# Optimization experiments

Measured on AMD Instinct MI355X. Metric: run time of the kernel, lower is better.

Reference implementation:

```python
import jax, jax.numpy as jnp
import numpy as np

N, E, DIM, H = 50000, 800000, 64, 2
HD = H * DIM


def setup_inputs() -> dict:
    key = jax.random.key(0)
    ks = jax.random.split(key, 16)
    s = 0.05
    return {
        "x": jax.random.normal(ks[0], (N, DIM), jnp.float32),
        "edge_index": jax.random.randint(ks[1], (2, E), 0, N, jnp.int64),
        "Wq": jax.random.normal(ks[2], (DIM, HD), jnp.float32) * s,
        "bq": jax.random.normal(ks[3], (HD,), jnp.float32) * s,
        "Wk": jax.random.normal(ks[4], (DIM, HD), jnp.float32) * s,
        "bk": jax.random.normal(ks[5], (HD,), jnp.float32) * s,
        "Wv": jax.random.normal(ks[6], (DIM, HD), jnp.float32) * s,
        "bv": jax.random.normal(ks[7], (HD,), jnp.float32) * s,
        "Wskip": jax.random.normal(ks[8], (DIM, HD), jnp.float32) * s,
        "bskip": jax.random.normal(ks[9], (HD,), jnp.float32) * s,
        "Wc": jax.random.normal(ks[10], (HD, DIM), jnp.float32) * s,
        "bc": jax.random.normal(ks[11], (DIM,), jnp.float32) * s,
        "gamma": jnp.ones((DIM,), jnp.float32),
        "beta": jnp.zeros((DIM,), jnp.float32),
    }


def reference(x, edge_index, Wq, bq, Wk, bk, Wv, bv, Wskip, bskip, Wc, bc, gamma, beta):
    src, dst = edge_index[0], edge_index[1]  # messages flow src -> dst
    # TransformerConv: per-head q/k/v projections, [N, H, D]
    q = (x @ Wq + bq).reshape(N, H, DIM)
    k = (x @ Wk + bk).reshape(N, H, DIM)
    v = (x @ Wv + bv).reshape(N, H, DIM)
    scale = 1.0 / np.sqrt(DIM).astype(np.float32)
    # edge-wise attention logits: [E, H]
    alpha = jnp.einsum('ehd,ehd->eh', q[dst], k[src]) * scale
    # segment softmax over incoming edges of each dst node (PyG softmax)
    amax = jax.ops.segment_max(alpha, dst, num_segments=N)
    a = jnp.exp(alpha - amax[dst])
    asum = jax.ops.segment_sum(a, dst, num_segments=N)
    a = a / (asum[dst] + 1e-16)
    # weighted scatter-aggregate of values: [N, H, D] -> concat heads
    out = jax.ops.segment_sum(a[:, :, None] * v[src], dst, num_segments=N)
    out = out.reshape(N, HD)
    # root/skip connection (root_weight=True default)
    out = out + (x @ Wskip + bskip)
    # concat linear: H*D -> dim
    out = out @ Wc + bc
    # pyg.LayerNorm default mode='graph': normalize over ALL nodes+features
    out = out - out.mean()
    out = out / (out.std() + 1e-5)  # std with unbiased=False (jnp default ddof=0)
    return out * gamma + beta
```

## Files before the change

### kernel.cpp

```cpp
#include <hip/hip_runtime.h>
#include <hip/hip_bf16.h>

#define N_NODES 50000
#define N_EDGES 800000
#define DIM 64
#define NHEAD 2
#define HD 128
#define NCOL 448
#define MAXDEG 64
#define DEGS 16

#define PREP_B 112
#define EDGE_B 3125
#define PROJ_B 782

typedef short bf16x8 __attribute__((ext_vector_type(8)));
typedef float f32x16 __attribute__((ext_vector_type(16)));
typedef float f32x2 __attribute__((ext_vector_type(2)));

__device__ __forceinline__ unsigned short f2bf(float f) {
    unsigned u = __float_as_uint(f);
    unsigned r = (u + 0x7fffu + ((u >> 16) & 1u)) >> 16;
    return (unsigned short)r;
}
__device__ __forceinline__ unsigned char f2fp8(float f) {
    int r = __builtin_amdgcn_cvt_pk_fp8_f32(f, f, 0, false);
    return (unsigned char)(r & 0xff);
}

__global__ __launch_bounds__(256) void k_prep(
    const float* __restrict__ Wq, const float* __restrict__ bq,
    const float* __restrict__ Wk, const float* __restrict__ bk,
    const float* __restrict__ Wv, const float* __restrict__ bv,
    const float* __restrict__ Wskip, const float* __restrict__ bskip,
    const float* __restrict__ Wc, const float* __restrict__ bc,
    unsigned short* __restrict__ WallT, float* __restrict__ ball,
    double* __restrict__ stats)
{
    int gid = blockIdx.x * 256 + threadIdx.x;
    if (gid == 0) { stats[0] = 0.0; stats[1] = 0.0; }
    const int j = gid >> 6;
    const int d = gid & 63;
    float w, bb;
    if (j < 128) {
        w = Wq[d * HD + j] * 0.125f;
        bb = bq[j] * 0.125f;
    } else if (j < 256) {
        int jj = j - 128;
        w = Wk[d * HD + jj];
        bb = bk[jj];
    } else if (j < 384) {
        int jj = j - 256;
        int h = jj >> 6, jc = jj & 63;
        float s = 0.f, sb = 0.f;
        for (int c = 0; c < 64; c++) {
            float wc = Wc[(h * 64 + c) * DIM + jc];
            s  += Wv[d * HD + h * 64 + c] * wc;
            sb += bv[h * 64 + c] * wc;
        }
        w = s; bb = sb;
    } else {
        int jj = j - 384;
        float s = 0.f, sb = bc[jj];
        for (int c = 0; c < HD; c++) {
            float wc = Wc[c * DIM + jj];
            s  += Wskip[d * HD + c] * wc;
            sb += bskip[c] * wc;
        }
        w = s; bb = sb;
    }
    WallT[gid] = f2bf(w);
    if (d == 0) ball[j] = bb;
}

__global__ __launch_bounds__(256) void k_ep(
    const float* __restrict__ x, const int* __restrict__ ei,
    const unsigned short* __restrict__ WallT, const float* __restrict__ ball,
    float* __restrict__ q, unsigned char* __restrict__ kv, float* __restrict__ skipc,
    int* __restrict__ deg, int* __restrict__ elist)
{
    const int blk = blockIdx.x;
    const int t = threadIdx.x;
    if (blk >= PROJ_B) {
        int gid = (blk - PROJ_B) * 256 + t;
        int src = ei[gid];
        int d   = ei[N_EDGES + gid];
        int pos = atomicAdd(&deg[(size_t)d * DEGS], 1);
        if (pos < MAXDEG) elist[(size_t)d * MAXDEG + pos] = src;
        return;
    }
    const int w = t >> 6;
    const int lane = t & 63;
    const int col = lane & 31;
    const int khalf = lane >> 5;
    const int n0 = blk * 64 + (w >> 1) * 32;
    const int ct0 = (w & 1) * 7;
    const int rowbase = 4 * khalf;

    int nread = n0 + col; if (nread >= N_NODES) nread = N_NODES - 1;
    const float* ap = x + (size_t)nread * 64 + khalf * 8;
    bf16x8 afrag[4];
#pragma unroll
    for (int kk = 0; kk < 4; kk++) {
        float4 xa = *((const float4*)(ap + kk * 16));
        float4 xb4 = *((const float4*)(ap + kk * 16 + 4));
        bf16x8 f;
        f[0] = (short)f2bf(xa.x); f[1] = (short)f2bf(xa.y);
        f[2] = (short)f2bf(xa.z); f[3] = (short)f2bf(xa.w);
        f[4] = (short)f2bf(xb4.x); f[5] = (short)f2bf(xb4.y);
        f[6] = (short)f2bf(xb4.z); f[7] = (short)f2bf(xb4.w);
        afrag[kk] = f;
    }

    for (int tt = 0; tt < 7; tt++) {
        const int gc = (ct0 + tt) * 32 + col;
        const float b = ball[gc];
        f32x16 acc;
#pragma unroll
        for (int r = 0; r < 16; r++) acc[r] = b;
        const unsigned short* bp = WallT + (size_t)gc * 64 + khalf * 8;
#pragma unroll
        for (int kk = 0; kk < 4; kk++) {
            bf16x8 bfrag = *((const bf16x8*)(bp + kk * 16));
            acc = __builtin_amdgcn_mfma_f32_32x32x16_bf16(afrag[kk], bfrag, acc, 0, 0, 0);
        }
        if (gc < 128) {
#pragma unroll
            for (int r = 0; r < 16; r++) {
                int node = n0 + (r & 3) + 8 * (r >> 2) + rowbase;
                if (node < N_NODES) q[(size_t)node * HD + gc] = acc[r];
            }
        } else if (gc < 384) {
            int ch = gc - 128;
#pragma unroll
            for (int r = 0; r < 16; r++) {
                int node = n0 + (r & 3) + 8 * (r >> 2) + rowbase;
                if (node < N_NODES) kv[(size_t)node * 256 + ch] = f2fp8(acc[r]);
            }
        } else {
#pragma unroll
            for (int r = 0; r < 16; r++) {
                int node = n0 + (r & 3) + 8 * (r >> 2) + rowbase;
                if (node < N_NODES) skipc[(size_t)node * DIM + (gc - 384)] = acc[r];
            }
        }
    }
}

__global__ __launch_bounds__(256) void k_attn(
    const float* __restrict__ q, const unsigned char* __restrict__ kv,
    const float* __restrict__ skipc,
    const int* __restrict__ deg, const int* __restrict__ elist,
    float* __restrict__ out, float* __restrict__ parts)
{
    const int w = threadIdx.x >> 6;
    const int lane = threadIdx.x & 63;
    const int g = lane >> 3;
    const int j = lane & 7;
    const int n = blockIdx.x * 4 + w;
    const float4* qp = (const float4*)(q + (size_t)n * HD);
    const float4 qa = qp[2 * j],      qb = qp[2 * j + 1];
    const float4 qc = qp[16 + 2 * j], qd = qp[17 + 2 * j];
    float acc0[8], acc1[8];
#pragma unroll
    for (int i = 0; i < 8; i++) { acc0[i] = 0.f; acc1[i] = 0.f; }
    float l0 = 0.f, l1 = 0.f;
    const int start = n * MAXDEG;
    int dg = deg[(size_t)n * DEGS]; if (dg > MAXDEG) dg = MAXDEG;
    const int end = start + dg;
    for (int b0 = start; b0 < end; b0 += 8) {
        int idx = b0 + g;
        bool valid = idx < end;
        int s = elist[valid ? idx : start];
        const uint2* kp = (const uint2*)(kv + (size_t)s * 256);
        uint2 K0 = kp[j], K1 = kp[8 + j];
        uint2 V0 = kp[16 + j], V1 = kp[24 + j];
        f32x2 k0a = __builtin_amdgcn_cvt_pk_f32_fp8(K0.x, false);
        f32x2 k0b = __builtin_amdgcn_cvt_pk_f32_fp8(K0.x, true);
        f32x2 k0c = __builtin_amdgcn_cvt_pk_f32_fp8(K0.y, false);
        f32x2 k0d = __builtin_amdgcn_cvt_pk_f32_fp8(K0.y, true);
        f32x2 k1a = __builtin_amdgcn_cvt_pk_f32_fp8(K1.x, false);
        f32x2 k1b = __builtin_amdgcn_cvt_pk_f32_fp8(K1.x, true);
        f32x2 k1c = __builtin_amdgcn_cvt_pk_f32_fp8(K1.y, false);
        f32x2 k1d = __builtin_amdgcn_cvt_pk_f32_fp8(K1.y, true);
        float p0 = qa.x * k0a[0] + qa.y * k0a[1] + qa.z * k0b[0] + qa.w * k0b[1]
                 + qb.x * k0c[0] + qb.y * k0c[1] + qb.z * k0d[0] + qb.w * k0d[1];
        float p1 = qc.x * k1a[0] + qc.y * k1a[1] + qc.z * k1b[0] + qc.w * k1b[1]
                 + qd.x * k1c[0] + qd.y * k1c[1] + qd.z * k1d[0] + qd.w * k1d[1];
#pragma unroll
        for (int off = 1; off < 8; off <<= 1) {
            p0 += __shfl_xor(p0, off, 64);
            p1 += __shfl_xor(p1, off, 64);
        }
        float w0 = valid ? __expf(p0) : 0.f;
        float w1 = valid ? __expf(p1) : 0.f;
        l0 += w0; l1 += w1;
        f32x2 v0a = __builtin_amdgcn_cvt_pk_f32_fp8(V0.x, false);
        f32x2 v0b = __builtin_amdgcn_cvt_pk_f32_fp8(V0.x, true);
        f32x2 v0c = __builtin_amdgcn_cvt_pk_f32_fp8(V0.y, false);
        f32x2 v0d = __builtin_amdgcn_cvt_pk_f32_fp8(V0.y, true);
        f32x2 v1a = __builtin_amdgcn_cvt_pk_f32_fp8(V1.x, false);
        f32x2 v1b = __builtin_amdgcn_cvt_pk_f32_fp8(V1.x, true);
        f32x2 v1c = __builtin_amdgcn_cvt_pk_f32_fp8(V1.y, false);
        f32x2 v1d = __builtin_amdgcn_cvt_pk_f32_fp8(V1.y, true);
        acc0[0] += w0 * v0a[0]; acc0[1] += w0 * v0a[1];
        acc0[2] += w0 * v0b[0]; acc0[3] += w0 * v0b[1];
        acc0[4] += w0 * v0c[0]; acc0[5] += w0 * v0c[1];
        acc0[6] += w0 * v0d[0]; acc0[7] += w0 * v0d[1];
        acc1[0] += w1 * v1a[0]; acc1[1] += w1 * v1a[1];
        acc1[2] += w1 * v1b[0]; acc1[3] += w1 * v1b[1];
        acc1[4] += w1 * v1c[0]; acc1[5] += w1 * v1c[1];
        acc1[6] += w1 * v1d[0]; acc1[7] += w1 * v1d[1];
    }
#pragma unroll
    for (int off = 8; off < 64; off <<= 1) {
        l0 += __shfl_xor(l0, off, 64);
        l1 += __shfl_xor(l1, off, 64);
#pragma unroll
        for (int i = 0; i < 8; i++) {
            acc0[i] += __shfl_xor(acc0[i], off, 64);
            acc1[i] += __shfl_xor(acc1[i], off, 64);
        }
    }
    if (g == 0) {
        float inv0 = 1.f / (l0 + 1e-16f), inv1 = 1.f / (l1 + 1e-16f);
        const float4* sk = (const float4*)(skipc + (size_t)n * DIM);
        float4 sa = sk[2 * j], sb = sk[2 * j + 1];
        float o[8];
        o[0] = acc0[0] * inv0 + acc1[0] * inv1 + sa.x;
        o[1] = acc0[1] * inv0 + acc1[1] * inv1 + sa.y;
        o[2] = acc0[2] * inv0 + acc1[2] * inv1 + sa.z;
        o[3] = acc0[3] * inv0 + acc1[3] * inv1 + sa.w;
        o[4] = acc0[4] * inv0 + acc1[4] * inv1 + sb.x;
        o[5] = acc0[5] * inv0 + acc1[5] * inv1 + sb.y;
        o[6] = acc0[6] * inv0 + acc1[6] * inv1 + sb.z;
        o[7] = acc0[7] * inv0 + acc1[7] * inv1 + sb.w;
        float4 r0 = {o[0], o[1], o[2], o[3]}, r1 = {o[4], o[5], o[6], o[7]};
        float4* op = (float4*)(out + (size_t)n * DIM);
        op[2 * j] = r0; op[2 * j + 1] = r1;
        float s_ = 0.f, ss = 0.f;
#pragma unroll
        for (int i = 0; i < 8; i++) { s_ += o[i]; ss += o[i] * o[i]; }
#pragma unroll
        for (int off = 1; off < 8; off <<= 1) {
            s_ += __shfl_xor(s_, off, 64);
            ss += __shfl_xor(ss, off, 64);
        }
        if (j == 0) { parts[n * 2 + 0] = s_; parts[n * 2 + 1] = ss; }
    }
}

#define RED_BLOCKS 100
__global__ __launch_bounds__(256) void k_reduce(
    const float* __restrict__ parts, double* __restrict__ stats)
{
    double s = 0.0, ss = 0.0;
    for (int i = blockIdx.x * 256 + threadIdx.x; i < N_NODES; i += RED_BLOCKS * 256) {
        s  += (double)parts[i * 2 + 0];
        ss += (double)parts[i * 2 + 1];
    }
#pragma unroll
    for (int off = 32; off > 0; off >>= 1) {
        s  += __shfl_down(s, off);
        ss += __shfl_down(ss, off);
    }
    __shared__ double sdd[8];
    int wave = threadIdx.x >> 6;
    if ((threadIdx.x & 63) == 0) { sdd[wave * 2] = s; sdd[wave * 2 + 1] = ss; }
    __syncthreads();
    if (threadIdx.x == 0) {
        double S = 0.0, SS = 0.0;
        for (int w = 0; w < 4; w++) { S += sdd[w * 2]; SS += sdd[w * 2 + 1]; }
        atomicAdd(&stats[0], S);
        atomicAdd(&stats[1], SS);
    }
}

__global__ __launch_bounds__(256) void k_norm(
    float* __restrict__ out, const double* __restrict__ stats,
    const float* __restrict__ gamma, const float* __restrict__ beta)
{
    int i = blockIdx.x * 256 + threadIdx.x;
    if (i >= N_NODES * DIM / 4) return;
    const double cnt = (double)N_NODES * (double)DIM;
    double mean = stats[0] / cnt;
    double var  = stats[1] / cnt - mean * mean;
    if (var < 0.0) var = 0.0;
    float mf = (float)mean;
    float inv = 1.0f / ((float)sqrt(var) + 1e-5f);
    float4 v = ((const float4*)out)[i];
    float4 gv = ((const float4*)gamma)[i & 15];
    float4 bv2 = ((const float4*)beta)[i & 15];
    v.x = (v.x - mf) * inv * gv.x + bv2.x;
    v.y = (v.y - mf) * inv * gv.y + bv2.y;
    v.z = (v.z - mf) * inv * gv.z + bv2.z;
    v.w = (v.w - mf) * inv * gv.w + bv2.w;
    ((float4*)out)[i] = v;
}

extern "C" void kernel_launch(void* const* d_in, const int* in_sizes, int n_in,
                              void* d_out, int out_size, void* d_ws, size_t ws_size,
                              hipStream_t stream) {
    const float* x     = (const float*)d_in[0];
    const int*   ei    = (const int*)d_in[1];
    const float* Wq    = (const float*)d_in[2];
    const float* bq    = (const float*)d_in[3];
    const float* Wk    = (const float*)d_in[4];
    const float* bk    = (const float*)d_in[5];
    const float* Wv    = (const float*)d_in[6];
    const float* bv    = (const float*)d_in[7];
    const float* Wsk   = (const float*)d_in[8];
    const float* bsk   = (const float*)d_in[9];
    const float* Wc    = (const float*)d_in[10];
    const float* bc    = (const float*)d_in[11];
    const float* gamma = (const float*)d_in[12];
    const float* beta  = (const float*)d_in[13];
    float* out = (float*)d_out;

    float* ws = (float*)d_ws;
    const size_t NF = (size_t)N_NODES * HD;
    float* q = ws;
    unsigned char* kv = (unsigned char*)(ws + NF);
    float* skipc = (float*)(kv + (size_t)N_NODES * 256);
    unsigned short* WallT = (unsigned short*)(skipc + (size_t)N_NODES * DIM);
    float* ball   = (float*)(WallT + NCOL * 64);
    int* deg      = (int*)(ball + NCOL);
    int* elist    = deg + (size_t)N_NODES * DEGS;
    float* parts  = (float*)(elist + (size_t)N_NODES * MAXDEG);
    double* stats = (double*)(parts + (size_t)N_NODES * 2);

    hipMemsetAsync(deg, 0, (size_t)N_NODES * DEGS * sizeof(int), stream);
    hipLaunchKernelGGL(k_prep, dim3(PREP_B), dim3(256), 0, stream,
                       Wq, bq, Wk, bk, Wv, bv, Wsk, bsk, Wc, bc, WallT, ball, stats);
    hipLaunchKernelGGL(k_ep, dim3(PROJ_B + EDGE_B), dim3(256), 0, stream,
                       x, ei, WallT, ball, q, kv, skipc, deg, elist);
    hipLaunchKernelGGL(k_attn, dim3(N_NODES / 4), dim3(256), 0, stream,
                       q, kv, skipc, deg, elist, out, parts);
    hipLaunchKernelGGL(k_reduce, dim3(RED_BLOCKS), dim3(256), 0, stream, parts, stats);
    hipLaunchKernelGGL(k_norm, dim3(N_NODES * DIM / 4 / 256 + 1), dim3(256), 0, stream,
                       out, stats, gamma, beta);
}
```

Before: 200.1 us.

## Replace global-atomic edge scatter with two-pass binned counting sort by destination

Edges are first partitioned into 256-node destination bins by a new kernel that sorts each edge chunk locally in shared memory and reserves bin space with one global atomic per bin. The edge part of the projection kernel then builds per-node adjacency lists from each bin using shared-memory atomics and writes a compact degree array. This removes the per-edge global atomics on padded degree counters and the degree memset. In exchange it adds a kernel launch and an intermediate bin buffer, and packs src into 16 bits and caps each bin at BCAP, relying on N below 65536 and bounded bin sizes.

Result: faster. 192.3 us (-3.9%).

```diff
diff --git a/kernel.cpp b/kernel.cpp
--- a/kernel.cpp
+++ b/kernel.cpp
@@ -8,10 +8,13 @@
 #define HD 128
 #define NCOL 448
 #define MAXDEG 64
-#define DEGS 16
+
+#define NBIN 196
+#define BCAP 6144
+#define ACH 4096
+#define ABLK 196
 
 #define PREP_B 112
-#define EDGE_B 3125
 #define PROJ_B 782
 
 typedef short bf16x8 __attribute__((ext_vector_type(8)));
@@ -35,10 +38,11 @@
     const float* __restrict__ Wskip, const float* __restrict__ bskip,
     const float* __restrict__ Wc, const float* __restrict__ bc,
     unsigned short* __restrict__ WallT, float* __restrict__ ball,
-    double* __restrict__ stats)
+    int* __restrict__ bincnt, double* __restrict__ stats)
 {
     int gid = blockIdx.x * 256 + threadIdx.x;
     if (gid == 0) { stats[0] = 0.0; stats[1] = 0.0; }
+    if (gid < NBIN) bincnt[gid] = 0;
     const int j = gid >> 6;
     const int d = gid & 63;
     float w, bb;
@@ -73,20 +77,99 @@
     if (d == 0) ball[j] = bb;
 }
 
+__global__ __launch_bounds__(256) void k_bin(
+    const int* __restrict__ ei, int* __restrict__ bincnt,
+    unsigned* __restrict__ bins)
+{
+    __shared__ unsigned pk[ACH];
+    __shared__ unsigned char bbn[ACH];
+    __shared__ unsigned ord[ACH];
+    __shared__ int hist[256];
+    __shared__ int lofs[256];
+    __shared__ int gbase[256];
+    const int t = threadIdx.x;
+    const int e0 = blockIdx.x * ACH;
+    for (int i = t; i < 256; i += 256) hist[i] = 0;
+    __syncthreads();
+    for (int i = t; i < ACH; i += 256) {
+        int e = e0 + i;
+        if (e < N_EDGES) {
+            int src = ei[e];
+            int d = ei[N_EDGES + e];
+            int bin = d >> 8;
+            pk[i] = (unsigned)(((d & 255) << 16) | src);
+            bbn[i] = (unsigned char)bin;
+            atomicAdd(&hist[bin], 1);
+        } else {
+            bbn[i] = 255;
+        }
+    }
+    __syncthreads();
+    int h = hist[t];
+    lofs[t] = h;
+    __syncthreads();
+    for (int off = 1; off < 256; off <<= 1) {
+        int add = (t >= off) ? lofs[t - off] : 0;
+        __syncthreads();
+        lofs[t] += add;
+        __syncthreads();
+    }
+    int excl = lofs[t] - h;
+    if (t < NBIN && h > 0) gbase[t] = atomicAdd(&bincnt[t], h);
+    __syncthreads();
+    lofs[t] = excl;
+    hist[t] = 0;
+    __syncthreads();
+    for (int i = t; i < ACH; i += 256) {
+        int bin = bbn[i];
+        if (bin != 255) {
+            int sl = atomicAdd(&hist[bin], 1);
+            ord[lofs[bin] + sl] = pk[i];
+        }
+    }
+    __syncthreads();
+    const int w = t >> 6, lane = t & 63;
+    for (int bin = w; bin < NBIN; bin += 4) {
+        int cnt = hist[bin];
+        int lo = lofs[bin];
+        int gb = gbase[bin];
+        for (int i = lane; i < cnt; i += 64) {
+            int pos = gb + i;
+            if (pos < BCAP) bins[(size_t)bin * BCAP + pos] = ord[lo + i];
+        }
+    }
+}
+
 __global__ __launch_bounds__(256) void k_ep(
-    const float* __restrict__ x, const int* __restrict__ ei,
+    const float* __restrict__ x,
     const unsigned short* __restrict__ WallT, const float* __restrict__ ball,
     float* __restrict__ q, unsigned char* __restrict__ kv, float* __restrict__ skipc,
+    const int* __restrict__ bincnt, const unsigned* __restrict__ bins,
     int* __restrict__ deg, int* __restrict__ elist)
 {
     const int blk = blockIdx.x;
     const int t = threadIdx.x;
     if (blk >= PROJ_B) {
-        int gid = (blk - PROJ_B) * 256 + t;
-        int src = ei[gid];
-        int d   = ei[N_EDGES + gid];
-        int pos = atomicAdd(&deg[(size_t)d * DEGS], 1);
-        if (pos < MAXDEG) elist[(size_t)d * MAXDEG + pos] = src;
+        const int bin = blk - PROJ_B;
+        __shared__ int nodecnt[256];
+        nodecnt[t] = 0;
+        __syncthreads();
+        int cnt = bincnt[bin]; if (cnt > BCAP) cnt = BCAP;
+        const unsigned* bp = bins + (size_t)bin * BCAP;
+        for (int i = t; i < cnt; i += 256) {
+            unsigned p = bp[i];
+            int local = p >> 16;
+            int src = p & 0xffff;
+            int sl = atomicAdd(&nodecnt[local], 1);
+            if (sl < MAXDEG)
+                elist[((size_t)((bin << 8) | local)) * MAXDEG + sl] = src;
+        }
+        __syncthreads();
+        int node = (bin << 8) + t;
+        if (node < N_NODES) {
+            int dgv = nodecnt[t];
+            deg[node] = dgv > MAXDEG ? MAXDEG : dgv;
+        }
         return;
     }
     const int w = t >> 6;
@@ -166,7 +249,7 @@
     for (int i = 0; i < 8; i++) { acc0[i] = 0.f; acc1[i] = 0.f; }
     float l0 = 0.f, l1 = 0.f;
     const int start = n * MAXDEG;
-    int dg = deg[(size_t)n * DEGS]; if (dg > MAXDEG) dg = MAXDEG;
+    int dg = deg[n]; if (dg > MAXDEG) dg = MAXDEG;
     const int end = start + dg;
     for (int b0 = start; b0 < end; b0 += 8) {
         int idx = b0 + g;
@@ -324,16 +407,19 @@
     float* skipc = (float*)(kv + (size_t)N_NODES * 256);
     unsigned short* WallT = (unsigned short*)(skipc + (size_t)N_NODES * DIM);
     float* ball   = (float*)(WallT + NCOL * 64);
-    int* deg      = (int*)(ball + NCOL);
-    int* elist    = deg + (size_t)N_NODES * DEGS;
+    int* bincnt   = (int*)(ball + NCOL);
+    unsigned* bins = (unsigned*)(bincnt + 256);
+    int* deg      = (int*)(bins + (size_t)NBIN * BCAP);
+    int* elist    = deg + N_NODES;
     float* parts  = (float*)(elist + (size_t)N_NODES * MAXDEG);
     double* stats = (double*)(parts + (size_t)N_NODES * 2);
 
-    hipMemsetAsync(deg, 0, (size_t)N_NODES * DEGS * sizeof(int), stream);
     hipLaunchKernelGGL(k_prep, dim3(PREP_B), dim3(256), 0, stream,
-                       Wq, bq, Wk, bk, Wv, bv, Wsk, bsk, Wc, bc, WallT, ball, stats);
-    hipLaunchKernelGGL(k_ep, dim3(PROJ_B + EDGE_B), dim3(256), 0, stream,
-                       x, ei, WallT, ball, q, kv, skipc, deg, elist);
+                       Wq, bq, Wk, bk, Wv, bv, Wsk, bsk, Wc, bc,
+                       WallT, ball, bincnt, stats);
+    hipLaunchKernelGGL(k_bin, dim3(ABLK), dim3(256), 0, stream, ei, bincnt, bins);
+    hipLaunchKernelGGL(k_ep, dim3(PROJ_B + NBIN), dim3(256), 0, stream,
+                       x, WallT, ball, q, kv, skipc, bincnt, bins, deg, elist);
     hipLaunchKernelGGL(k_attn, dim3(N_NODES / 4), dim3(256), 0, stream,
                        q, kv, skipc, deg, elist, out, parts);
     hipLaunchKernelGGL(k_reduce, dim3(RED_BLOCKS), dim3(256), 0, stream, parts, stats);
```
